# Kernel tuning notes

Hardware: AMD Instinct MI355X
Metric: run time of the kernel (lower is better)

Reference implementation:

```python
import jax, jax.numpy as jnp
import numpy as np

EPS = 1e-5


def _grid_edges(H, W):
    # radius_graph on the HxW integer grid with r=1.0, loop=False -> 4-neighbors,
    # then GCNConv's gcn_norm adds self-loops; we append them here once.
    idx = np.arange(H * W).reshape(H, W)
    r_s, r_d = idx[:, :-1].ravel(), idx[:, 1:].ravel()
    d_s, d_d = idx[:-1, :].ravel(), idx[1:, :].ravel()
    loop = np.arange(H * W)
    src = np.concatenate([r_s, r_d, d_s, d_d, loop])
    dst = np.concatenate([r_d, r_s, d_d, d_s, loop])
    return jnp.asarray(src, jnp.int32), jnp.asarray(dst, jnp.int32)


def _gcn_conv(x, W, b, src, dst, deg, dinv):
    # GCNConv(aggr='mean'): xw = x @ W; message = dinv[src]*dinv[dst] * xw[src];
    # mean-aggregate over incoming edges (incl. self-loop); add bias.
    xw = x @ W  # [B, N, Cout]
    w = (dinv[src] * dinv[dst])[None, :, None]
    agg = jnp.zeros((x.shape[0], x.shape[1], W.shape[1]), xw.dtype).at[:, dst].add(xw[:, src] * w)
    return agg / deg[None, :, None] + b


def _bn(x, gamma, beta):
    # BatchNorm2d, training-mode batch statistics (torch default), biased variance
    mu = x.mean(axis=(0, 2, 3), keepdims=True)
    var = ((x - mu) ** 2).mean(axis=(0, 2, 3), keepdims=True)
    return (x - mu) * jax.lax.rsqrt(var + EPS) * gamma[None, :, None, None] + beta[None, :, None, None]


def setup_inputs() -> dict:
    key = jax.random.key(0)
    ks = jax.random.split(key, 5)
    B, H, W, Cin, Cout = 8, 64, 64, 512, 512
    s = 0.02
    return {
        'x': jax.random.normal(ks[0], (B, H * W, Cin), jnp.float32),
        'H': H, 'W': W,
        'w_res': jax.random.normal(ks[1], (Cin, Cout), jnp.float32) * s,
        'w_pre': jax.random.normal(ks[2], (Cin, Cout), jnp.float32) * s,
        'b_pre': jnp.zeros((Cout,), jnp.float32),
        'w_g1': jax.random.normal(ks[3], (Cout, Cout), jnp.float32) * s,
        'b_g1': jnp.zeros((Cout,), jnp.float32),
        'w_g2': jax.random.normal(ks[4], (Cout, Cout), jnp.float32) * s,
        'b_g2': jnp.zeros((Cout,), jnp.float32),
        'g1': jnp.ones((Cout,), jnp.float32), 'beta1': jnp.zeros((Cout,), jnp.float32),
        'g2': jnp.ones((Cout,), jnp.float32), 'beta2': jnp.zeros((Cout,), jnp.float32),
    }


def reference(x, H, W, w_res, w_pre, b_pre, w_g1, b_g1, w_g2, b_g2, g1, beta1, g2, beta2):
    B, N, Cin = x.shape
    src, dst = _grid_edges(H, W)
    deg = jnp.zeros((N,), x.dtype).at[dst].add(1.0)  # in-degree incl. self-loops
    dinv = jax.lax.rsqrt(deg)
    # 1x1 convs on tokens == per-node matmuls
    residual = jnp.einsum('bnc,cd->bnd', x, w_res)
    xr = jnp.einsum('bnc,cd->bnd', x, w_pre) + b_pre
    h = jax.nn.relu(_gcn_conv(xr, w_g1, b_g1, src, dst, deg, dinv))
    h = jax.nn.relu(_gcn_conv(h, w_g2, b_g2, src, dst, deg, dinv))
    pooled = h.mean(axis=1)  # global_mean_pool -> [B, Cout]
    xg = _bn(pooled[:, :, None, None], g1, beta1)  # [B, Cout, 1, 1]
    res_img = residual.transpose(0, 2, 1).reshape(B, -1, H, W)
    return _bn(res_img + xg, g2, beta2)  # [B, Cout, H, W]
```

## Files before the change

### kernel.cpp

```cpp
#include <hip/hip_runtime.h>
#include <hip/hip_bf16.h>

using bf16 = __hip_bfloat16;
typedef __attribute__((ext_vector_type(8))) __bf16 bf16x8;
typedef __attribute__((ext_vector_type(4))) float f32x4;

__device__ __forceinline__ float bf2f(bf16 v) { return __bfloat162float(v); }
__device__ __forceinline__ bf16 f2bf(float f) { return __float2bfloat16(f); }

union bfu8 { bf16x8 v; bf16 h[8]; int4 i; };

__device__ __forceinline__ bool probeF32(const unsigned* probe) {
    return probe != nullptr && probe[0] == 0x3F800000u;
}
__device__ __forceinline__ float ldIn(const void* p, int i, bool f32) {
    return f32 ? ((const float*)p)[i] : bf2f(((const bf16*)p)[i]);
}

#define BATCH 8
#define GRID 64
#define NNODE 4096
#define CDIM 512
#define MROWS 32768
#define EPSBN 1e-5f

#define BM 128
#define BN 128
#define BK 32

__device__ __forceinline__ void gload16(bf16* lds, const bf16* g) {
    __builtin_amdgcn_global_load_lds(
        (const __attribute__((address_space(1))) unsigned int*)g,
        (__attribute__((address_space(3))) unsigned int*)lds, 16, 0, 0);
}

#define PIN() __builtin_amdgcn_sched_barrier(0)

__global__ __launch_bounds__(256) void gemm_lds(const bf16* __restrict__ A,
                                                const bf16* __restrict__ BT,
                                                bf16* __restrict__ C0,
                                                bf16* __restrict__ C1,
                                                const float* __restrict__ bias,
                                                int K)
{
    __shared__ __align__(16) bf16 lA[2][BM * BK];
    __shared__ __align__(16) bf16 lB[2][BN * BK];

    const int tid  = threadIdx.x;
    const int bm = blockIdx.x, bn = blockIdx.y;
    const int wave = tid >> 6, lane = tid & 63;
    const int wr = (wave >> 1) * 64, wc = (wave & 1) * 64;
    const int lrow = lane & 15, quad = lane >> 4;

    f32x4 acc[4][4] = {};

    const bf16* Abase = A  + (size_t)bm * BM * K;
    const bf16* Bbase = BT + (size_t)bn * BN * K;

    const int srow = wave * 32 + (lane >> 2);
    const int scol = (lane & 3) * 8;
    const bf16* gA0 = Abase + (size_t)srow * K + scol;
    const bf16* gA1 = Abase + (size_t)(srow + 16) * K + scol;
    const bf16* gB0 = Bbase + (size_t)srow * K + scol;
    const bf16* gB1 = Bbase + (size_t)(srow + 16) * K + scol;
    bf16* laBase = &lA[0][0];
    bf16* lbBase = &lB[0][0];
    const int wofs = wave * 1024;

#define STAGE(BUF, TILE) do {                                              \
        const size_t koff_ = (size_t)(TILE) * BK;                          \
        gload16(laBase + (BUF) * (BM * BK) + wofs,       gA0 + koff_);     \
        gload16(laBase + (BUF) * (BM * BK) + wofs + 512, gA1 + koff_);     \
        gload16(lbBase + (BUF) * (BN * BK) + wofs,       gB0 + koff_);     \
        gload16(lbBase + (BUF) * (BN * BK) + wofs + 512, gB1 + koff_);     \
    } while (0)

#define COMPUTE(BUF) do {                                                  \
        const bf16* pA_ = laBase + (BUF) * (BM * BK);                      \
        const bf16* pB_ = lbBase + (BUF) * (BN * BK);                      \
        bf16x8 af[4], bv[4];                                               \
        _Pragma("unroll")                                                  \
        for (int i = 0; i < 4; ++i)                                        \
            af[i] = *(const bf16x8*)(pA_ + (wr + i * 16 + lrow) * BK + quad * 8); \
        _Pragma("unroll")                                                  \
        for (int j = 0; j < 4; ++j)                                        \
            bv[j] = *(const bf16x8*)(pB_ + (wc + j * 16 + lrow) * BK + quad * 8); \
        _Pragma("unroll")                                                  \
        for (int i = 0; i < 4; ++i)                                        \
            _Pragma("unroll")                                              \
            for (int j = 0; j < 4; ++j)                                    \
                acc[i][j] = __builtin_amdgcn_mfma_f32_16x16x32_bf16(af[i], bv[j], acc[i][j], 0, 0, 0); \
    } while (0)

    const int NT = K / BK;

    STAGE(0, 0);
    int t = 0;
    for (; t + 3 < NT; t += 2) {
        STAGE(1, t + 1);
        asm volatile("s_waitcnt vmcnt(4)" ::: "memory");
        __builtin_amdgcn_s_barrier(); PIN();
        COMPUTE(0);
        PIN(); __builtin_amdgcn_s_barrier(); PIN();

        STAGE(0, t + 2);
        asm volatile("s_waitcnt vmcnt(4)" ::: "memory");
        __builtin_amdgcn_s_barrier(); PIN();
        COMPUTE(1);
        PIN(); __builtin_amdgcn_s_barrier(); PIN();
    }
    STAGE(1, t + 1);
    asm volatile("s_waitcnt vmcnt(4)" ::: "memory");
    __builtin_amdgcn_s_barrier(); PIN();
    COMPUTE(0);
    PIN(); __builtin_amdgcn_s_barrier(); PIN();
    asm volatile("s_waitcnt vmcnt(0)" ::: "memory");
    __builtin_amdgcn_s_barrier(); PIN();
    COMPUTE(1);

#undef STAGE
#undef COMPUTE

    #pragma unroll
    for (int i = 0; i < 4; ++i) {
        const int mbase = bm * BM + wr + i * 16 + quad * 4;
        #pragma unroll
        for (int j = 0; j < 4; ++j) {
            int n = bn * BN + wc + j * 16 + lrow;
            bf16* Cd = C0;
            float bvv = 0.0f;
            if (C1 != nullptr && n >= CDIM) { Cd = C1; n -= CDIM; }
            else if (bias != nullptr)       { bvv = bias[n]; }
            #pragma unroll
            for (int rr = 0; rr < 4; ++rr)
                Cd[(size_t)(mbase + rr) * CDIM + n] = f2bf(acc[i][j][rr] + bvv);
        }
    }
}

__global__ __launch_bounds__(256) void convertX(const void* __restrict__ x,
                                                bf16* __restrict__ xb,
                                                const unsigned* __restrict__ probe)
{
    const bool f32 = probeF32(probe);
    const size_t i = ((size_t)blockIdx.x * 256 + threadIdx.x) * 8;
    if (f32) {
        const float4 u0 = *(const float4*)((const float*)x + i);
        const float4 u1 = *(const float4*)((const float*)x + i + 4);
        bf16 t[8] = { f2bf(u0.x), f2bf(u0.y), f2bf(u0.z), f2bf(u0.w),
                      f2bf(u1.x), f2bf(u1.y), f2bf(u1.z), f2bf(u1.w) };
        *(int4*)(xb + i) = *(const int4*)t;
    } else {
        *(int4*)(xb + i) = *(const int4*)((const bf16*)x + i);
    }
}

__global__ __launch_bounds__(256) void weightPrep(const void* __restrict__ s0,
                                                  const void* __restrict__ s1,
                                                  const void* __restrict__ s2,
                                                  const void* __restrict__ s3,
                                                  bf16* __restrict__ dstBase,
                                                  const unsigned* __restrict__ probe)
{
    __shared__ float tile[64][65];
    const bool f32 = probeF32(probe);
    const int z = blockIdx.z;
    const void* src = (z == 0) ? s0 : (z == 1) ? s1 : (z == 2) ? s2 : s3;
    bf16* dst = dstBase + (size_t)(z + 1) * 512 * 512;
    const int bx = blockIdx.x, by = blockIdx.y;
    const int t = threadIdx.x;
    const int col = t & 63, rbase = t >> 6;

    if (z == 3) {
        #pragma unroll 4
        for (int i = 0; i < 16; ++i) {
            int r = i * 4 + rbase;
            size_t idx = (size_t)(by * 64 + r) * 512 + bx * 64 + col;
            dst[idx] = f2bf(ldIn(src, idx, f32));
        }
        return;
    }
    #pragma unroll 4
    for (int i = 0; i < 16; ++i) {
        int r = i * 4 + rbase;
        tile[r][col] = ldIn(src, (by * 64 + r) * 512 + bx * 64 + col, f32);
    }
    __syncthreads();
    #pragma unroll 4
    for (int i = 0; i < 16; ++i) {
        int r = i * 4 + rbase;
        dst[(size_t)(bx * 64 + r) * 512 + by * 64 + col] = f2bf(tile[col][r]);
    }
}

__global__ void bc1_kernel(const void* __restrict__ b_pre,
                           const bf16* __restrict__ BTg1,
                           const unsigned* __restrict__ probe,
                           float* __restrict__ bc1)
{
    const bool f32 = probeF32(probe);
    const int e = blockIdx.x * 256 + threadIdx.x;
    float s = 0.0f;
    for (int d0 = 0; d0 < 512; d0 += 8) {
        bfu8 u; u.v = *(const bf16x8*)(BTg1 + (size_t)e * 512 + d0);
        #pragma unroll
        for (int j = 0; j < 8; ++j)
            s += ldIn(b_pre, d0 + j, f32) * bf2f(u.h[j]);
    }
    bc1[e] = s;
}

__device__ __forceinline__ float degOf(int y, int x) {
    return 1.0f + (y > 0) + (y < GRID - 1) + (x > 0) + (x < GRID - 1);
}

__global__ __launch_bounds__(256) void gcn_agg_v2(const bf16* __restrict__ T,
                                                  const void* __restrict__ bias,
                                                  const unsigned* __restrict__ probe,
                                                  bf16* __restrict__ H)
{
    const bool f32 = probeF32(probe);
    const int t = threadIdx.x;
    const int lane = t & 63, sub = t >> 6;
    const int n = blockIdx.x * 4 + sub;
    const int b = blockIdx.y;
    const int y = n >> 6, x = n & 63;
    const int cg = lane * 8;

    const float deg = degOf(y, x);
    const float dn  = rsqrtf(deg);
    const float inv = dn / deg;

    const bf16* cptr = T + ((size_t)b * NNODE + n) * CDIM + cg;

    bfu8 vc; vc.v = *(const bf16x8*)cptr;
    float s[8];
    #pragma unroll
    for (int j = 0; j < 8; ++j) s[j] = dn * bf2f(vc.h[j]);

    if (y > 0)        { float d = rsqrtf(degOf(y - 1, x)); bfu8 u; u.v = *(const bf16x8*)(cptr - 64 * CDIM);
                        #pragma unroll
                        for (int j = 0; j < 8; ++j) s[j] += d * bf2f(u.h[j]); }
    if (y < GRID - 1) { float d = rsqrtf(degOf(y + 1, x)); bfu8 u; u.v = *(const bf16x8*)(cptr + 64 * CDIM);
                        #pragma unroll
                        for (int j = 0; j < 8; ++j) s[j] += d * bf2f(u.h[j]); }
    if (x > 0)        { float d = rsqrtf(degOf(y, x - 1)); bfu8 u; u.v = *(const bf16x8*)(cptr - CDIM);
                        #pragma unroll
                        for (int j = 0; j < 8; ++j) s[j] += d * bf2f(u.h[j]); }
    if (x < GRID - 1) { float d = rsqrtf(degOf(y, x + 1)); bfu8 u; u.v = *(const bf16x8*)(cptr + CDIM);
                        #pragma unroll
                        for (int j = 0; j < 8; ++j) s[j] += d * bf2f(u.h[j]); }

    bfu8 o;
    #pragma unroll
    for (int j = 0; j < 8; ++j)
        o.h[j] = f2bf(fmaxf(s[j] * inv + ldIn(bias, cg + j, f32), 0.0f));
    *(int4*)(H + ((size_t)b * NNODE + n) * CDIM + cg) = o.i;
}

__global__ __launch_bounds__(256) void gcn_agg_pool_v3(const bf16* __restrict__ T,
                                                       const void* __restrict__ bias,
                                                       const unsigned* __restrict__ probe,
                                                       float* __restrict__ poolPart)
{
    const bool f32 = probeF32(probe);
    const int y = blockIdx.x;
    const int b = blockIdx.y;
    const int t = threadIdx.x;
    const int lane = t & 63, sub = t >> 6;
    const int cg = lane * 8;

    const bf16* base = T + (size_t)b * NNODE * CDIM;

    float biasv[8];
    #pragma unroll
    for (int j = 0; j < 8; ++j) biasv[j] = ldIn(bias, cg + j, f32);

    float acc[8] = {};

    for (int xi = 0; xi < 16; ++xi) {
        const int x = sub * 16 + xi;
        const int n = y * 64 + x;
        const float deg = degOf(y, x);
        const float dn  = rsqrtf(deg);
        const float inv = dn / deg;
        const bf16* cptr = base + (size_t)n * CDIM + cg;

        bfu8 vc; vc.v = *(const bf16x8*)cptr;
        float s[8];
        #pragma unroll
        for (int j = 0; j < 8; ++j) s[j] = dn * bf2f(vc.h[j]);

        if (y > 0)        { float d = rsqrtf(degOf(y - 1, x)); bfu8 u; u.v = *(const bf16x8*)(cptr - 64 * CDIM);
                            #pragma unroll
                            for (int j = 0; j < 8; ++j) s[j] += d * bf2f(u.h[j]); }
        if (y < GRID - 1) { float d = rsqrtf(degOf(y + 1, x)); bfu8 u; u.v = *(const bf16x8*)(cptr + 64 * CDIM);
                            #pragma unroll
                            for (int j = 0; j < 8; ++j) s[j] += d * bf2f(u.h[j]); }
        if (x > 0)        { float d = rsqrtf(degOf(y, x - 1)); bfu8 u; u.v = *(const bf16x8*)(cptr - CDIM);
                            #pragma unroll
                            for (int j = 0; j < 8; ++j) s[j] += d * bf2f(u.h[j]); }
        if (x < GRID - 1) { float d = rsqrtf(degOf(y, x + 1)); bfu8 u; u.v = *(const bf16x8*)(cptr + CDIM);
                            #pragma unroll
                            for (int j = 0; j < 8; ++j) s[j] += d * bf2f(u.h[j]); }

        #pragma unroll
        for (int j = 0; j < 8; ++j)
            acc[j] += fmaxf(s[j] * inv + biasv[j], 0.0f);
    }

    __shared__ float red[4][64][9];
    #pragma unroll
    for (int j = 0; j < 8; ++j) red[sub][lane][j] = acc[j];
    __syncthreads();
    if (sub == 0) {
        float* dst = poolPart + (size_t)(b * GRID + y) * CDIM + cg;
        #pragma unroll
        for (int j = 0; j < 8; ++j)
            dst[j] = red[0][lane][j] + red[1][lane][j] + red[2][lane][j] + red[3][lane][j];
    }
}

__global__ void bn1_kernel(const float* __restrict__ poolPart,
                           const void* __restrict__ g1, const void* __restrict__ beta1,
                           const unsigned* __restrict__ probe,
                           float* __restrict__ xg)
{
    const bool f32 = probeF32(probe);
    const int c = blockIdx.x * 256 + threadIdx.x;
    float p[BATCH];
    float mu = 0.0f;
    #pragma unroll
    for (int b = 0; b < BATCH; ++b) {
        float a0 = 0, a1 = 0, a2 = 0, a3 = 0;
        const float* src = poolPart + (size_t)b * GRID * CDIM + c;
        #pragma unroll 4
        for (int y = 0; y < GRID; y += 4) {
            a0 += src[(size_t)(y + 0) * CDIM];
            a1 += src[(size_t)(y + 1) * CDIM];
            a2 += src[(size_t)(y + 2) * CDIM];
            a3 += src[(size_t)(y + 3) * CDIM];
        }
        p[b] = (a0 + a1 + a2 + a3) * (1.0f / (float)NNODE);
        mu += p[b];
    }
    mu *= (1.0f / (float)BATCH);
    float var = 0.0f;
    #pragma unroll
    for (int b = 0; b < BATCH; ++b) { float d = p[b] - mu; var += d * d; }
    var *= (1.0f / (float)BATCH);
    const float rs = rsqrtf(var + EPSBN) * ldIn(g1, c, f32);
    const float bt = ldIn(beta1, c, f32);
    #pragma unroll
    for (int b = 0; b < BATCH; ++b)
        xg[b * CDIM + c] = (p[b] - mu) * rs + bt;
}

__global__ __launch_bounds__(256) void bn2_stats_part(const bf16* __restrict__ R,
                                                      const float* __restrict__ xg,
                                                      float* __restrict__ bn2Part)
{
    const int t = threadIdx.x;
    const int lane = t & 63, sub = t >> 6;
    const int cg = lane * 8;
    const int row0 = blockIdx.x * 128;
    const int b = row0 >> 12;

    float xgv[8];
    #pragma unroll
    for (int j = 0; j < 8; ++j) xgv[j] = xg[b * CDIM + cg + j];

    float s[8] = {}, q[8] = {};
    #pragma unroll
    for (int i0 = 0; i0 < 4; ++i0) {
        const bf16* base = R + (size_t)(row0 + i0 * 32 + sub * 8) * CDIM + cg;
        #pragma unroll
        for (int k = 0; k < 8; ++k) {
            bfu8 u; u.v = *(const bf16x8*)(base + (size_t)k * CDIM);
            #pragma unroll
            for (int j = 0; j < 8; ++j) {
                float v = bf2f(u.h[j]) + xgv[j];
                s[j] += v; q[j] += v * v;
            }
        }
    }

    __shared__ float redS[4][64][9], redQ[4][64][9];
    #pragma unroll
    for (int j = 0; j < 8; ++j) { redS[sub][lane][j] = s[j]; redQ[sub][lane][j] = q[j]; }
    __syncthreads();
    if (sub == 0) {
        float* dst = bn2Part + (size_t)blockIdx.x * 1024;
        #pragma unroll
        for (int j = 0; j < 8; ++j) {
            dst[cg + j]       = redS[0][lane][j] + redS[1][lane][j] + redS[2][lane][j] + redS[3][lane][j];
            dst[512 + cg + j] = redQ[0][lane][j] + redQ[1][lane][j] + redQ[2][lane][j] + redQ[3][lane][j];
        }
    }
}

__global__ void bn2_reduce(const float* __restrict__ bn2Part, float* __restrict__ sums)
{
    const int c = blockIdx.x * 256 + threadIdx.x;
    float a0 = 0, a1 = 0, a2 = 0, a3 = 0, a4 = 0, a5 = 0, a6 = 0, a7 = 0;
    #pragma unroll 4
    for (int blk = 0; blk < 256; blk += 8) {
        a0 += bn2Part[(size_t)(blk + 0) * 1024 + c];
        a1 += bn2Part[(size_t)(blk + 1) * 1024 + c];
        a2 += bn2Part[(size_t)(blk + 2) * 1024 + c];
        a3 += bn2Part[(size_t)(blk + 3) * 1024 + c];
        a4 += bn2Part[(size_t)(blk + 4) * 1024 + c];
        a5 += bn2Part[(size_t)(blk + 5) * 1024 + c];
        a6 += bn2Part[(size_t)(blk + 6) * 1024 + c];
        a7 += bn2Part[(size_t)(blk + 7) * 1024 + c];
    }
    sums[c] = ((a0 + a1) + (a2 + a3)) + ((a4 + a5) + (a6 + a7));
}

__global__ void bn2_final(const float* __restrict__ sums, const float* __restrict__ xg,
                          const void* __restrict__ g2, const void* __restrict__ beta2,
                          const unsigned* __restrict__ probe,
                          float* __restrict__ scale, float* __restrict__ tshift)
{
    const bool f32 = probeF32(probe);
    const int c = blockIdx.x * 256 + threadIdx.x;
    const float mu  = sums[c] * (1.0f / (float)MROWS);
    const float var = sums[512 + c] * (1.0f / (float)MROWS) - mu * mu;
    const float sc  = ldIn(g2, c, f32) * rsqrtf(var + EPSBN);
    scale[c] = sc;
    const float base = ldIn(beta2, c, f32) - mu * sc;
    #pragma unroll
    for (int b = 0; b < BATCH; ++b)
        tshift[b * CDIM + c] = xg[b * CDIM + c] * sc + base;
}

__global__ __launch_bounds__(256) void out_transpose(const bf16* __restrict__ R,
                                                     const float* __restrict__ scale,
                                                     const float* __restrict__ tshift,
                                                     const unsigned* __restrict__ probe,
                                                     void* __restrict__ outv)
{
    __shared__ float tile[64][65];
    const bool f32 = probeF32(probe);
    const int nt = blockIdx.x;
    const int ct = blockIdx.y;
    const int b  = blockIdx.z;
    const int t = threadIdx.x;
    const int c0 = ct * 64, n0 = nt * 64;

    const int rr  = t >> 3;
    const int cch = (t & 7) * 8;
    #pragma unroll
    for (int half = 0; half < 2; ++half) {
        int r = rr + half * 32;
        bfu8 u; u.v = *(const bf16x8*)(R + ((size_t)(b * NNODE + n0 + r)) * CDIM + c0 + cch);
        #pragma unroll
        for (int j = 0; j < 8; ++j) tile[r][cch + j] = bf2f(u.h[j]);
    }
    __syncthreads();

    const int col = t & 63, rbase = t >> 6;
    if (f32) {
        float* out = (float*)outv;
        #pragma unroll 4
        for (int i = 0; i < 16; ++i) {
            int cc = i * 4 + rbase;
            float sc  = scale[c0 + cc];
            float tsh = tshift[b * CDIM + c0 + cc];
            out[((size_t)(b * CDIM + c0 + cc)) * NNODE + n0 + col] = tile[col][cc] * sc + tsh;
        }
    } else {
        bf16* out = (bf16*)outv;
        #pragma unroll 4
        for (int i = 0; i < 16; ++i) {
            int cc = i * 4 + rbase;
            float sc  = scale[c0 + cc];
            float tsh = tshift[b * CDIM + c0 + cc];
            out[((size_t)(b * CDIM + c0 + cc)) * NNODE + n0 + col] = f2bf(tile[col][cc] * sc + tsh);
        }
    }
}

extern "C" void kernel_launch(void* const* d_in, const int* in_sizes, int n_in,
                              void* d_out, int out_size, void* d_ws, size_t ws_size,
                              hipStream_t stream)
{
    const void* x     = d_in[0];
    const void* w_res = d_in[3];
    const void* w_pre = d_in[4];
    const void* b_pre = d_in[5];
    const void* w_g1  = d_in[6];
    const void* b_g1  = d_in[7];
    const void* w_g2  = d_in[8];
    const void* b_g2  = d_in[9];
    const void* g1    = d_in[10];
    const void* beta1 = d_in[11];
    const void* g2    = d_in[12];
    const void* beta2 = d_in[13];
    const unsigned* probe = (const unsigned*)g1;

    char* ws = (char*)d_ws;
    constexpr size_t WSZ = (size_t)512 * 512 * 2;

    bf16* BTc1  = (bf16*)(ws);
    bf16* BTres = (bf16*)(ws + WSZ);
    bf16* BTg1  = (bf16*)(ws + 2 * WSZ);
    bf16* BTg2  = (bf16*)(ws + 3 * WSZ);
    bf16* Wpre_b= (bf16*)(ws + 4 * WSZ);
    char* smallb = ws + 5 * WSZ;
    float* sums   = (float*)(smallb);
    float* xg     = (float*)(smallb + 4096);
    float* scale  = (float*)(smallb + 4096 + 16384);
    float* tshift = (float*)(smallb + 4096 + 16384 + 2048);
    float* bc1    = (float*)(smallb + 4096 + 16384 + 2048 + 16384);
    bf16* Rres = (bf16*)(smallb + 65536);

    char* dA = (char*)d_out;
    char* dB = (char*)d_out + (size_t)MROWS * CDIM * 2;

    bf16* Ta = (bf16*)dA;
    bf16* Xb = (bf16*)dB;
    float* poolPart = (float*)dB;
    float* bn2Part  = (float*)(dB + (1 << 20));

    dim3 blk(256);

    weightPrep<<<dim3(8, 8, 4), blk, 0, stream>>>(w_res, w_g1, w_g2, w_pre,
                                                  (bf16*)ws, probe);
    convertX<<<dim3(MROWS * CDIM / (256 * 8)), blk, 0, stream>>>(x, Xb, probe);
    gemm_lds<<<dim3(512 / BM, 512 / BN), blk, 0, stream>>>(BTg1, Wpre_b, BTc1,
                                                           nullptr, nullptr, CDIM);
    bc1_kernel<<<dim3(2), blk, 0, stream>>>(b_pre, BTg1, probe, bc1);
    gemm_lds<<<dim3(MROWS / BM, 1024 / BN), blk, 0, stream>>>(Xb, BTc1, Ta, Rres, bc1, CDIM);
    gcn_agg_v2<<<dim3(NNODE / 4, BATCH), blk, 0, stream>>>(Ta, b_g1, probe, Xb);
    gemm_lds<<<dim3(MROWS / BM, CDIM / BN), blk, 0, stream>>>(Xb, BTg2, Ta, nullptr, nullptr, CDIM);
    gcn_agg_pool_v3<<<dim3(GRID, BATCH), blk, 0, stream>>>(Ta, b_g2, probe, poolPart);
    bn1_kernel<<<dim3(2), blk, 0, stream>>>(poolPart, g1, beta1, probe, xg);
    bn2_stats_part<<<dim3(MROWS / 128), blk, 0, stream>>>(Rres, xg, bn2Part);
    bn2_reduce<<<dim3(4), blk, 0, stream>>>(bn2Part, sums);
    bn2_final<<<dim3(2), blk, 0, stream>>>(sums, xg, g2, beta2, probe, scale, tshift);
    out_transpose<<<dim3(NNODE / 64, CDIM / 64, BATCH), blk, 0, stream>>>(Rres, scale, tshift, probe, d_out);
}
```

Baseline: 406.4 us.

## Triple-buffer GEMM LDS pipeline and vectorize epilogue stores via swapped MFMA operands

Moves the GEMM main loop from a double-buffered to a triple-buffered LDS pipeline. Tiles are prefetched two steps ahead, and the trailing barrier's sched pin is dropped, so global loads get more time to land before compute. The MFMA operands are also swapped so each lane holds four consecutive output columns. This lets the epilogue write 8-byte vector stores with a float4 bias load instead of scalar strided stores. The cost is 50% more shared memory per block, which may lower occupancy.

After: 419.2 us. 1.03x slower.

```diff
diff --git a/kernel.cpp b/kernel.cpp
--- a/kernel.cpp
+++ b/kernel.cpp
@@ -9,6 +9,7 @@
 __device__ __forceinline__ bf16 f2bf(float f) { return __float2bfloat16(f); }
 
 union bfu8 { bf16x8 v; bf16 h[8]; int4 i; };
+union bfu4 { bf16 h[4]; uint2 u; };
 
 __device__ __forceinline__ bool probeF32(const unsigned* probe) {
     return probe != nullptr && probe[0] == 0x3F800000u;
@@ -43,8 +44,8 @@
                                                 const float* __restrict__ bias,
                                                 int K)
 {
-    __shared__ __align__(16) bf16 lA[2][BM * BK];
-    __shared__ __align__(16) bf16 lB[2][BN * BK];
+    __shared__ __align__(16) bf16 lA[3][BM * BK];
+    __shared__ __align__(16) bf16 lB[3][BN * BK];
 
     const int tid  = threadIdx.x;
     const int bm = blockIdx.x, bn = blockIdx.y;
@@ -89,51 +90,50 @@
         for (int i = 0; i < 4; ++i)                                        \
             _Pragma("unroll")                                              \
             for (int j = 0; j < 4; ++j)                                    \
-                acc[i][j] = __builtin_amdgcn_mfma_f32_16x16x32_bf16(af[i], bv[j], acc[i][j], 0, 0, 0); \
+                acc[i][j] = __builtin_amdgcn_mfma_f32_16x16x32_bf16(bv[j], af[i], acc[i][j], 0, 0, 0); \
     } while (0)
 
     const int NT = K / BK;
 
     STAGE(0, 0);
-    int t = 0;
-    for (; t + 3 < NT; t += 2) {
-        STAGE(1, t + 1);
-        asm volatile("s_waitcnt vmcnt(4)" ::: "memory");
+    STAGE(1, 1);
+    for (int t = 0; t < NT; ++t) {
+        const int cb = t % 3;
+        if (t + 2 < NT) {
+            STAGE((t + 2) % 3, t + 2);
+            asm volatile("s_waitcnt vmcnt(8)" ::: "memory");
+        } else if (t + 2 == NT) {
+            asm volatile("s_waitcnt vmcnt(4)" ::: "memory");
+        } else {
+            asm volatile("s_waitcnt vmcnt(0)" ::: "memory");
+        }
         __builtin_amdgcn_s_barrier(); PIN();
-        COMPUTE(0);
-        PIN(); __builtin_amdgcn_s_barrier(); PIN();
-
-        STAGE(0, t + 2);
-        asm volatile("s_waitcnt vmcnt(4)" ::: "memory");
-        __builtin_amdgcn_s_barrier(); PIN();
-        COMPUTE(1);
-        PIN(); __builtin_amdgcn_s_barrier(); PIN();
-    }
-    STAGE(1, t + 1);
-    asm volatile("s_waitcnt vmcnt(4)" ::: "memory");
-    __builtin_amdgcn_s_barrier(); PIN();
-    COMPUTE(0);
-    PIN(); __builtin_amdgcn_s_barrier(); PIN();
-    asm volatile("s_waitcnt vmcnt(0)" ::: "memory");
-    __builtin_amdgcn_s_barrier(); PIN();
-    COMPUTE(1);
+        COMPUTE(cb);
+        PIN(); __builtin_amdgcn_s_barrier();
+    }
 
 #undef STAGE
 #undef COMPUTE
 
+    const bool toC1 = (C1 != nullptr) && (bn >= CDIM / BN);
+    bf16* Cd = toC1 ? C1 : C0;
+    const bool addB = (!toC1) && (bias != nullptr);
+    const int nbase = (toC1 ? (bn - CDIM / BN) : bn) * BN + wc + quad * 4;
+    const int mrow0 = bm * BM + wr + lrow;
     #pragma unroll
     for (int i = 0; i < 4; ++i) {
-        const int mbase = bm * BM + wr + i * 16 + quad * 4;
+        const int m = mrow0 + i * 16;
         #pragma unroll
         for (int j = 0; j < 4; ++j) {
-            int n = bn * BN + wc + j * 16 + lrow;
-            bf16* Cd = C0;
-            float bvv = 0.0f;
-            if (C1 != nullptr && n >= CDIM) { Cd = C1; n -= CDIM; }
-            else if (bias != nullptr)       { bvv = bias[n]; }
-            #pragma unroll
-            for (int rr = 0; rr < 4; ++rr)
-                Cd[(size_t)(mbase + rr) * CDIM + n] = f2bf(acc[i][j][rr] + bvv);
+            const int n0 = nbase + j * 16;
+            float4 bv4 = make_float4(0.f, 0.f, 0.f, 0.f);
+            if (addB) bv4 = *(const float4*)(bias + n0);
+            bfu4 o;
+            o.h[0] = f2bf(acc[i][j][0] + bv4.x);
+            o.h[1] = f2bf(acc[i][j][1] + bv4.y);
+            o.h[2] = f2bf(acc[i][j][2] + bv4.z);
+            o.h[3] = f2bf(acc[i][j][3] + bv4.w);
+            *(uint2*)(Cd + (size_t)m * CDIM + n0) = o.u;
         }
     }
 }
```

## Fuse BN2 per-batch statistics into residual GEMM epilogue with atomics

Applied to the files above, without the earlier changes.

The residual GEMM epilogue now accumulates per-batch, per-channel sums and sums of squares of the rounded outputs. It reduces them across lanes with shuffles and LDS, then atomically adds them into a small buffer. The separate bn2_stats_part and bn2_reduce kernels, which re-read the full residual tensor, are removed. The final kernel expands the xg shift algebraically from the per-batch sums. The MFMA operand order is also swapped so each lane holds 4 consecutive columns, which allows vectorized 8-byte stores and float4 bias loads. The cost is extra epilogue work, atomics and a memset. E[x^2]-mu^2 is already used, so the precision risk is similar to before.

Measured after the change: 472.9 us. 1.16x slower.

```diff
diff --git a/kernel.cpp b/kernel.cpp
--- a/kernel.cpp
+++ b/kernel.cpp
@@ -9,6 +9,7 @@
 __device__ __forceinline__ bf16 f2bf(float f) { return __float2bfloat16(f); }
 
 union bfu8 { bf16x8 v; bf16 h[8]; int4 i; };
+union bfu4 { bf16 h[4]; uint2 u; };
 
 __device__ __forceinline__ bool probeF32(const unsigned* probe) {
     return probe != nullptr && probe[0] == 0x3F800000u;
@@ -41,10 +42,13 @@
                                                 bf16* __restrict__ C0,
                                                 bf16* __restrict__ C1,
                                                 const float* __restrict__ bias,
+                                                float* __restrict__ Sb,
+                                                float* __restrict__ Qb,
                                                 int K)
 {
     __shared__ __align__(16) bf16 lA[2][BM * BK];
     __shared__ __align__(16) bf16 lB[2][BN * BK];
+    __shared__ float statS[4][4][16], statQ[4][4][16];
 
     const int tid  = threadIdx.x;
     const int bm = blockIdx.x, bn = blockIdx.y;
@@ -89,7 +93,7 @@
         for (int i = 0; i < 4; ++i)                                        \
             _Pragma("unroll")                                              \
             for (int j = 0; j < 4; ++j)                                    \
-                acc[i][j] = __builtin_amdgcn_mfma_f32_16x16x32_bf16(af[i], bv[j], acc[i][j], 0, 0, 0); \
+                acc[i][j] = __builtin_amdgcn_mfma_f32_16x16x32_bf16(bv[j], af[i], acc[i][j], 0, 0, 0); \
     } while (0)
 
     const int NT = K / BK;
@@ -121,19 +125,69 @@
 #undef STAGE
 #undef COMPUTE
 
+    const bool toC1 = (C1 != nullptr) && (bn >= CDIM / BN);
+    bf16* Cd = toC1 ? C1 : C0;
+    const bool addB = (!toC1) && (bias != nullptr);
+    const int nbase = (toC1 ? (bn - CDIM / BN) : bn) * BN + wc + quad * 4;
+    const int mrow0 = bm * BM + wr + lrow;
+    const bool doStats = toC1 && (Sb != nullptr);
+
+    float sAcc[16], qAcc[16];
+    #pragma unroll
+    for (int k = 0; k < 16; ++k) { sAcc[k] = 0.0f; qAcc[k] = 0.0f; }
+
     #pragma unroll
     for (int i = 0; i < 4; ++i) {
-        const int mbase = bm * BM + wr + i * 16 + quad * 4;
+        const int m = mrow0 + i * 16;
         #pragma unroll
         for (int j = 0; j < 4; ++j) {
-            int n = bn * BN + wc + j * 16 + lrow;
-            bf16* Cd = C0;
-            float bvv = 0.0f;
-            if (C1 != nullptr && n >= CDIM) { Cd = C1; n -= CDIM; }
-            else if (bias != nullptr)       { bvv = bias[n]; }
+            const int n0 = nbase + j * 16;
+            float4 bv4 = make_float4(0.f, 0.f, 0.f, 0.f);
+            if (addB) bv4 = *(const float4*)(bias + n0);
+            bfu4 o;
+            o.h[0] = f2bf(acc[i][j][0] + bv4.x);
+            o.h[1] = f2bf(acc[i][j][1] + bv4.y);
+            o.h[2] = f2bf(acc[i][j][2] + bv4.z);
+            o.h[3] = f2bf(acc[i][j][3] + bv4.w);
+            if (doStats) {
+                #pragma unroll
+                for (int rr = 0; rr < 4; ++rr) {
+                    float r = bf2f(o.h[rr]);
+                    sAcc[j * 4 + rr] += r;
+                    qAcc[j * 4 + rr] += r * r;
+                }
+            }
+            *(uint2*)(Cd + (size_t)m * CDIM + n0) = o.u;
+        }
+    }
+
+    if (doStats) {
+        #pragma unroll
+        for (int k = 0; k < 16; ++k) {
             #pragma unroll
-            for (int rr = 0; rr < 4; ++rr)
-                Cd[(size_t)(mbase + rr) * CDIM + n] = f2bf(acc[i][j][rr] + bvv);
+            for (int msk = 1; msk < 16; msk <<= 1) {
+                sAcc[k] += __shfl_xor(sAcc[k], msk);
+                qAcc[k] += __shfl_xor(qAcc[k], msk);
+            }
+        }
+        if (lrow == 0) {
+            #pragma unroll
+            for (int k = 0; k < 16; ++k) {
+                statS[wave][quad][k] = sAcc[k];
+                statQ[wave][quad][k] = qAcc[k];
+            }
+        }
+        __syncthreads();
+        if (tid < 128) {
+            const int col = tid;
+            const int wcb = col >> 6, q = (col >> 2) & 3;
+            const int slot = ((col >> 4) & 3) * 4 + (col & 3);
+            const float S = statS[wcb][q][slot] + statS[wcb + 2][q][slot];
+            const float Q = statQ[wcb][q][slot] + statQ[wcb + 2][q][slot];
+            const int b = (bm * BM) >> 12;
+            const int c = (bn - CDIM / BN) * BN + col;
+            atomicAdd(&Sb[b * CDIM + c], S);
+            atomicAdd(&Qb[b * CDIM + c], Q);
         }
     }
 }
@@ -356,76 +410,24 @@
         xg[b * CDIM + c] = (p[b] - mu) * rs + bt;
 }
 
-__global__ __launch_bounds__(256) void bn2_stats_part(const bf16* __restrict__ R,
-                                                      const float* __restrict__ xg,
-                                                      float* __restrict__ bn2Part)
-{
-    const int t = threadIdx.x;
-    const int lane = t & 63, sub = t >> 6;
-    const int cg = lane * 8;
-    const int row0 = blockIdx.x * 128;
-    const int b = row0 >> 12;
-
-    float xgv[8];
-    #pragma unroll
-    for (int j = 0; j < 8; ++j) xgv[j] = xg[b * CDIM + cg + j];
-
-    float s[8] = {}, q[8] = {};
-    #pragma unroll
-    for (int i0 = 0; i0 < 4; ++i0) {
-        const bf16* base = R + (size_t)(row0 + i0 * 32 + sub * 8) * CDIM + cg;
-        #pragma unroll
-        for (int k = 0; k < 8; ++k) {
-            bfu8 u; u.v = *(const bf16x8*)(base + (size_t)k * CDIM);
-            #pragma unroll
-            for (int j = 0; j < 8; ++j) {
-                float v = bf2f(u.h[j]) + xgv[j];
-                s[j] += v; q[j] += v * v;
-            }
-        }
-    }
-
-    __shared__ float redS[4][64][9], redQ[4][64][9];
-    #pragma unroll
-    for (int j = 0; j < 8; ++j) { redS[sub][lane][j] = s[j]; redQ[sub][lane][j] = q[j]; }
-    __syncthreads();
-    if (sub == 0) {
-        float* dst = bn2Part + (size_t)blockIdx.x * 1024;
-        #pragma unroll
-        for (int j = 0; j < 8; ++j) {
-            dst[cg + j]       = redS[0][lane][j] + redS[1][lane][j] + redS[2][lane][j] + redS[3][lane][j];
-            dst[512 + cg + j] = redQ[0][lane][j] + redQ[1][lane][j] + redQ[2][lane][j] + redQ[3][lane][j];
-        }
-    }
-}
-
-__global__ void bn2_reduce(const float* __restrict__ bn2Part, float* __restrict__ sums)
-{
+__global__ void bn2_final2(const float* __restrict__ Sb, const float* __restrict__ Qb,
+                           const float* __restrict__ xg,
+                           const void* __restrict__ g2, const void* __restrict__ beta2,
+                           const unsigned* __restrict__ probe,
+                           float* __restrict__ scale, float* __restrict__ tshift)
+{
+    const bool f32 = probeF32(probe);
     const int c = blockIdx.x * 256 + threadIdx.x;
-    float a0 = 0, a1 = 0, a2 = 0, a3 = 0, a4 = 0, a5 = 0, a6 = 0, a7 = 0;
-    #pragma unroll 4
-    for (int blk = 0; blk < 256; blk += 8) {
-        a0 += bn2Part[(size_t)(blk + 0) * 1024 + c];
-        a1 += bn2Part[(size_t)(blk + 1) * 1024 + c];
-        a2 += bn2Part[(size_t)(blk + 2) * 1024 + c];
-        a3 += bn2Part[(size_t)(blk + 3) * 1024 + c];
-        a4 += bn2Part[(size_t)(blk + 4) * 1024 + c];
-        a5 += bn2Part[(size_t)(blk + 5) * 1024 + c];
-        a6 += bn2Part[(size_t)(blk + 6) * 1024 + c];
-        a7 += bn2Part[(size_t)(blk + 7) * 1024 + c];
-    }
-    sums[c] = ((a0 + a1) + (a2 + a3)) + ((a4 + a5) + (a6 + a7));
-}
-
-__global__ void bn2_final(const float* __restrict__ sums, const float* __restrict__ xg,
-                          const void* __restrict__ g2, const void* __restrict__ beta2,
-                          const unsigned* __restrict__ probe,
-                          float* __restrict__ scale, float* __restrict__ tshift)
-{
-    const bool f32 = probeF32(probe);
-    const int c = blockIdx.x * 256 + threadIdx.x;
-    const float mu  = sums[c] * (1.0f / (float)MROWS);
-    const float var = sums[512 + c] * (1.0f / (float)MROWS) - mu * mu;
+    float sAll = 0.0f, qAll = 0.0f;
+    #pragma unroll
+    for (int b = 0; b < BATCH; ++b) {
+        const float s   = Sb[b * CDIM + c];
+        const float xgv = xg[b * CDIM + c];
+        sAll += s + (float)NNODE * xgv;
+        qAll += Qb[b * CDIM + c] + 2.0f * xgv * s + (float)NNODE * xgv * xgv;
+    }
+    const float mu  = sAll * (1.0f / (float)MROWS);
+    const float var = qAll * (1.0f / (float)MROWS) - mu * mu;
     const float sc  = ldIn(g2, c, f32) * rsqrtf(var + EPSBN);
     scale[c] = sc;
     const float base = ldIn(beta2, c, f32) - mu * sc;
@@ -507,12 +509,13 @@
     bf16* BTg1  = (bf16*)(ws + 2 * WSZ);
     bf16* BTg2  = (bf16*)(ws + 3 * WSZ);
     bf16* Wpre_b= (bf16*)(ws + 4 * WSZ);
+    float* Sb   = (float*)(ws + 4 * WSZ);
+    float* Qb   = (float*)(ws + 4 * WSZ + 16384);
     char* smallb = ws + 5 * WSZ;
-    float* sums   = (float*)(smallb);
-    float* xg     = (float*)(smallb + 4096);
-    float* scale  = (float*)(smallb + 4096 + 16384);
-    float* tshift = (float*)(smallb + 4096 + 16384 + 2048);
-    float* bc1    = (float*)(smallb + 4096 + 16384 + 2048 + 16384);
+    float* xg     = (float*)(smallb);
+    float* scale  = (float*)(smallb + 16384);
+    float* tshift = (float*)(smallb + 16384 + 2048);
+    float* bc1    = (float*)(smallb + 16384 + 2048 + 16384);
     bf16* Rres = (bf16*)(smallb + 65536);
 
     char* dA = (char*)d_out;
@@ -521,7 +524,6 @@
     bf16* Ta = (bf16*)dA;
     bf16* Xb = (bf16*)dB;
     float* poolPart = (float*)dB;
-    float* bn2Part  = (float*)(dB + (1 << 20));
 
     dim3 blk(256);
 
@@ -529,15 +531,18 @@
                                                   (bf16*)ws, probe);
     convertX<<<dim3(MROWS * CDIM / (256 * 8)), blk, 0, stream>>>(x, Xb, probe);
     gemm_lds<<<dim3(512 / BM, 512 / BN), blk, 0, stream>>>(BTg1, Wpre_b, BTc1,
+                                                           nullptr, nullptr,
                                                            nullptr, nullptr, CDIM);
     bc1_kernel<<<dim3(2), blk, 0, stream>>>(b_pre, BTg1, probe, bc1);
-    gemm_lds<<<dim3(MROWS / BM, 1024 / BN), blk, 0, stream>>>(Xb, BTc1, Ta, Rres, bc1, CDIM);
+    hipMemsetAsync(Sb, 0, 2 * 16384, stream);
+    gemm_lds<<<dim3(MROWS / BM, 1024 / BN), blk, 0, stream>>>(Xb, BTc1, Ta, Rres,
+                                                              bc1, Sb, Qb, CDIM);
     gcn_agg_v2<<<dim3(NNODE / 4, BATCH), blk, 0, stream>>>(Ta, b_g1, probe, Xb);
-    gemm_lds<<<dim3(MROWS / BM, CDIM / BN), blk, 0, stream>>>(Xb, BTg2, Ta, nullptr, nullptr, CDIM);
+    gemm_lds<<<dim3(MROWS / BM, CDIM / BN), blk, 0, stream>>>(Xb, BTg2, Ta, nullptr,
+                                                              nullptr, nullptr,
+                                                              nullptr, CDIM);
     gcn_agg_pool_v3<<<dim3(GRID, BATCH), blk, 0, stream>>>(Ta, b_g2, probe, poolPart);
     bn1_kernel<<<dim3(2), blk, 0, stream>>>(poolPart, g1, beta1, probe, xg);
-    bn2_stats_part<<<dim3(MROWS / 128), blk, 0, stream>>>(Rres, xg, bn2Part);
-    bn2_reduce<<<dim3(4), blk, 0, stream>>>(bn2Part, sums);
-    bn2_final<<<dim3(2), blk, 0, stream>>>(sums, xg, g2, beta2, probe, scale, tshift);
+    bn2_final2<<<dim3(2), blk, 0, stream>>>(Sb, Qb, xg, g2, beta2, probe, scale, tshift);
     out_transpose<<<dim3(NNODE / 64, CDIM / 64, BATCH), blk, 0, stream>>>(Rres, scale, tshift, probe, d_out);
 }
```
